# Kernel tuning notes

Measured on AMD Instinct MI355X. Metric: run time of the kernel, lower is better.

Reference implementation:

```python
import jax, jax.numpy as jnp
import numpy as np

THRESHOLD = 0.1  # matches init kwarg 'threshold'


def setup_inputs() -> dict:
    key = jax.random.key(0)
    ks = jax.random.split(key, 4)
    B, T, D = 16, 4096, 1024   # batch, tokens(=patch_h*patch_w), d_model
    E, R = 8, 64               # experts, lora rank
    inputs = jax.random.normal(ks[0], (B, T, D), dtype=jnp.float32)
    gate_w = jax.random.normal(ks[1], (D, E), dtype=jnp.float32) * (1.0 / np.sqrt(D))
    gate_b = jnp.zeros((E,), dtype=jnp.float32)
    lora_A = jax.random.normal(ks[2], (E, D, R), dtype=jnp.float32) * (1.0 / np.sqrt(D))
    lora_B = jax.random.normal(ks[3], (E, R, D), dtype=jnp.float32) * (1.0 / np.sqrt(R))
    return {"inputs": inputs, "gate_w": gate_w, "gate_b": gate_b,
            "lora_A": lora_A, "lora_B": lora_B, "patch_h": 64, "patch_w": 64}


def reference(inputs, gate_w, gate_b, lora_A, lora_B, patch_h, patch_w):
    # patch_h / patch_w are unused by 'linear' LoRA experts (kept for signature parity)
    D = inputs.shape[-1]
    x = inputs.reshape(-1, D)                                  # [N, D]
    gate_logits = jax.nn.softmax(x @ gate_w + gate_b, axis=-1)  # [N, E]
    selected = (gate_logits >= THRESHOLD).astype(x.dtype)       # threshold gate
    weights = gate_logits * selected
    wsum = jnp.sum(weights, axis=-1, keepdims=True)
    wsum = jnp.where(wsum == 0, jnp.ones_like(wsum), wsum)
    weights = weights / wsum                                    # renormalized weights [N, E]
    # Dense equivalent of per-expert gather/scatter: tokens with weight 0 contribute nothing,
    # identical to the boolean-indexed accumulation in the torch code.
    h = jnp.einsum('nd,edr->ner', x, lora_A)                    # [N, E, R]
    out = jnp.einsum('ner,erd,ne->nd', h, lora_B, weights)      # weighted combine [N, D]
    return out.reshape(inputs.shape[:-1] + (D,))
```

## Files before the change

kernel.cpp:

```cpp
#include <hip/hip_runtime.h>
#include <stdint.h>
#include <stddef.h>


typedef float f32x4 __attribute__((ext_vector_type(4)));
typedef short bf16x8 __attribute__((ext_vector_type(8)));

#define MFMA_16x16x32(A, B, C) __builtin_amdgcn_mfma_f32_16x16x32_bf16((A), (B), (C), 0, 0, 0)
#define SCHED_FENCE() __builtin_amdgcn_sched_barrier(0)
#define BAR() __builtin_amdgcn_s_barrier()
#define WAIT_LGKM0() asm volatile("s_waitcnt lgkmcnt(0)" ::: "memory")
#define WAIT_VM3() asm volatile("s_waitcnt vmcnt(3)" ::: "memory")
#define WAIT_VM0_LGKM0() asm volatile("s_waitcnt vmcnt(0) lgkmcnt(0)" ::: "memory")
#define WAIT_VM0() asm volatile("s_waitcnt vmcnt(0)" ::: "memory")

__device__ __forceinline__ unsigned short f2bf(float f) {
    union { float f; unsigned int u; } v;
    v.f = f;
    unsigned int u = v.u;
    u += 0x7FFFu + ((u >> 16) & 1u);
    return (unsigned short)(u >> 16);
}

__device__ __forceinline__ void load16_lds(unsigned short* lds, const unsigned short* g) {
    __builtin_amdgcn_global_load_lds(
        (const __attribute__((address_space(1))) unsigned int*)g,
        (__attribute__((address_space(3))) unsigned int*)lds, 16, 0, 0);
}

__global__ __launch_bounds__(256) void convert_pack(
        const float* __restrict__ LA, const float* __restrict__ LB,
        unsigned short* __restrict__ A_P, unsigned short* __restrict__ B_P) {
    int gid = blockIdx.x * 256 + threadIdx.x;
    if (gid < 524288) {
        int j = gid & 7, l = (gid >> 3) & 63, cblk = (gid >> 9) & 31, kblk = gid >> 14;
        int d = kblk * 32 + (l >> 4) * 8 + j;
        int col = cblk * 16 + (l & 15);
        int e = col >> 6, r = col & 63;
        A_P[gid] = f2bf(LA[((size_t)e * 1024 + d) * 64 + r]);
    } else {
        int idx = gid - 524288;
        int j = idx & 7, l = (idx >> 3) & 63, cblk = (idx >> 9) & 63, kblk = idx >> 15;
        int k = kblk * 32 + (l >> 4) * 8 + j;
        int d = cblk * 16 + (l & 15);
        int e = k >> 6, r = k & 63;
        B_P[idx] = f2bf(LB[((size_t)e * 64 + r) * 1024 + d]);
    }
}

__global__ __launch_bounds__(256) void gate_kernel(
        const float* __restrict__ X, const float* __restrict__ GW,
        const float* __restrict__ GB, float* __restrict__ Wg) {
    __shared__ float gwt[8 * 1024];
    int tid = threadIdx.x;

    {
        float r[4][8];
#pragma unroll
        for (int j = 0; j < 4; ++j) {
            const f32x4* gp = (const f32x4*)(GW + (size_t)(tid * 4 + j) * 8);
            f32x4 g0 = gp[0], g1 = gp[1];
#pragma unroll
            for (int q = 0; q < 4; ++q) { r[j][q] = g0[q]; r[j][4 + q] = g1[q]; }
        }
#pragma unroll
        for (int e = 0; e < 8; ++e) {
            f32x4 v;
#pragma unroll
            for (int j = 0; j < 4; ++j) v[j] = r[j][e];
            *(f32x4*)&gwt[e * 1024 + tid * 4] = v;
        }
    }
    __syncthreads();

    int row = blockIdx.x * 16 + (tid >> 4);
    int sub = tid & 15;
    const float* xr = X + (size_t)row * 1024 + sub * 4;
    float lg[8];
#pragma unroll
    for (int e = 0; e < 8; ++e) lg[e] = 0.f;
#pragma unroll 4
    for (int it = 0; it < 16; ++it) {
        f32x4 x = *(const f32x4*)(xr + it * 64);
#pragma unroll
        for (int e = 0; e < 8; ++e) {
            f32x4 g = *(const f32x4*)&gwt[e * 1024 + it * 64 + sub * 4];
            lg[e] += x[0] * g[0];
            lg[e] += x[1] * g[1];
            lg[e] += x[2] * g[2];
            lg[e] += x[3] * g[3];
        }
    }
#pragma unroll
    for (int s = 1; s < 16; s <<= 1) {
#pragma unroll
        for (int e = 0; e < 8; ++e) lg[e] += __shfl_xor(lg[e], s, 16);
    }
    float p[8], m = -1e30f, ssum = 0.f;
#pragma unroll
    for (int e = 0; e < 8; ++e) { lg[e] += GB[e]; m = fmaxf(m, lg[e]); }
#pragma unroll
    for (int e = 0; e < 8; ++e) { p[e] = expf(lg[e] - m); ssum += p[e]; }
    float inv = 1.f / ssum;
    float wv[8], wsum = 0.f;
#pragma unroll
    for (int e = 0; e < 8; ++e) {
        float pe = p[e] * inv;
        wv[e] = (pe >= 0.1f) ? pe : 0.f;
        wsum += wv[e];
    }
    if (wsum == 0.f) wsum = 1.f;
    float invw = 1.f / wsum;
    if (sub < 8) Wg[(size_t)row * 8 + sub] = wv[sub] * invw;
}

__global__ __launch_bounds__(512, 4) void stage1_kernel(
        const float* __restrict__ X, const unsigned short* __restrict__ A_P,
        const float* __restrict__ Wg, unsigned short* __restrict__ H_P) {
    __shared__ union SM1 {
        struct {
            unsigned short a[2][32 * 512];
            unsigned short x[2][64 * 40];
        } p;
        unsigned short hb[64 * 520];
    } sm;
    __shared__ float wl[512];

    int tid = threadIdx.x;
    int lane = tid & 63;
    int w = tid >> 6;
    int blk = blockIdx.x;
    int row = tid >> 3;
    int sub = tid & 7;

    wl[tid] = Wg[(size_t)blk * 512 + tid];

    const float* xp = X + (size_t)blk * 64 * 1024 + (size_t)row * 1024 + sub * 4;
    unsigned short* aCur = sm.p.a[0];
    unsigned short* aNxt = sm.p.a[1];
    unsigned short* xCur = sm.p.x[0];
    unsigned short* xNxt = sm.p.x[1];

    {
        const unsigned short* asrc = A_P + tid * 8;
#pragma unroll
        for (int i = 0; i < 4; ++i)
            load16_lds(&aCur[tid * 8 + i * 4096], asrc + i * 4096);
    }
    SCHED_FENCE();
    f32x4 xv0 = *(const f32x4*)(xp);
    f32x4 xv_hold = *(const f32x4*)(xp + 32);
    {
        unsigned int lo = (unsigned int)f2bf(xv0[0]) | ((unsigned int)f2bf(xv0[1]) << 16);
        unsigned int hi = (unsigned int)f2bf(xv0[2]) | ((unsigned int)f2bf(xv0[3]) << 16);
        *((uint2*)&xCur[row * 40 + sub * 4]) = make_uint2(lo, hi);
    }

    f32x4 acc[4][4] = {};
    for (int kb = 0; kb < 31; ++kb) {
        const unsigned short* asrc = A_P + (size_t)(kb + 1) * 16384 + tid * 8;
#pragma unroll
        for (int i = 0; i < 4; ++i)
            load16_lds(&aNxt[tid * 8 + i * 4096], asrc + i * 4096);
        SCHED_FENCE();
        int kbn = (kb + 2 <= 31) ? kb + 2 : 31;
        f32x4 xv_new = *(const f32x4*)(xp + (size_t)kbn * 32);
        unsigned int lo = (unsigned int)f2bf(xv_hold[0]) | ((unsigned int)f2bf(xv_hold[1]) << 16);
        unsigned int hi = (unsigned int)f2bf(xv_hold[2]) | ((unsigned int)f2bf(xv_hold[3]) << 16);
        *((uint2*)&xNxt[row * 40 + sub * 4]) = make_uint2(lo, hi);
        WAIT_LGKM0();
        SCHED_FENCE();
        BAR();
        SCHED_FENCE();
        bf16x8 af[4], bv[4];
#pragma unroll
        for (int m = 0; m < 4; ++m)
            af[m] = *(const bf16x8*)&xCur[(m * 16 + (lane & 15)) * 40 + (lane >> 4) * 8];
#pragma unroll
        for (int n = 0; n < 4; ++n)
            bv[n] = *(const bf16x8*)&aCur[(w * 4 + n) * 512 + lane * 8];
#pragma unroll
        for (int m = 0; m < 4; ++m)
#pragma unroll
            for (int n = 0; n < 4; ++n)
                acc[m][n] = MFMA_16x16x32(af[m], bv[n], acc[m][n]);
        BAR();
        unsigned short* t;
        t = aCur; aCur = aNxt; aNxt = t;
        t = xCur; xCur = xNxt; xNxt = t;
        xv_hold = xv_new;
    }
    WAIT_VM0_LGKM0();
    SCHED_FENCE();
    BAR();
    SCHED_FENCE();
    {
        bf16x8 af[4], bv[4];
#pragma unroll
        for (int m = 0; m < 4; ++m)
            af[m] = *(const bf16x8*)&xCur[(m * 16 + (lane & 15)) * 40 + (lane >> 4) * 8];
#pragma unroll
        for (int n = 0; n < 4; ++n)
            bv[n] = *(const bf16x8*)&aCur[(w * 4 + n) * 512 + lane * 8];
#pragma unroll
        for (int m = 0; m < 4; ++m)
#pragma unroll
            for (int n = 0; n < 4; ++n)
                acc[m][n] = MFMA_16x16x32(af[m], bv[n], acc[m][n]);
    }
    __syncthreads();

#pragma unroll
    for (int m = 0; m < 4; ++m) {
        float wv[4];
#pragma unroll
        for (int r = 0; r < 4; ++r)
            wv[r] = wl[(m * 16 + (lane >> 4) * 4 + r) * 8 + w];
#pragma unroll
        for (int n = 0; n < 4; ++n) {
            int col = w * 64 + n * 16 + (lane & 15);
#pragma unroll
            for (int r = 0; r < 4; ++r) {
                int rr = m * 16 + (lane >> 4) * 4 + r;
                sm.hb[rr * 520 + col] = f2bf(acc[m][n][r] * wv[r]);
            }
        }
    }
    __syncthreads();
#pragma unroll
    for (int it = 0; it < 8; ++it) {
        int gi = tid + it * 512;
        int ft = gi >> 6;
        int l2 = gi & 63;
        int rowblk = ft >> 4;
        int kblk = ft & 15;
        int rr = rowblk * 16 + (l2 & 15);
        int cs = kblk * 32 + (l2 >> 4) * 8;
        uint4 v = *(const uint4*)&sm.hb[rr * 520 + cs];
        *(uint4*)&H_P[(((size_t)blk * 4 + rowblk) * 16 + kblk) * 512 + l2 * 8] = v;
    }
}

__global__ __launch_bounds__(512, 4) void stage2_kernel(
        const unsigned short* __restrict__ H_P, const unsigned short* __restrict__ B_P,
        float* __restrict__ Out) {
    __shared__ unsigned short a_lds[2][8 * 512];
    __shared__ unsigned short b_lds[2][16 * 512];

    int tid = threadIdx.x;
    int lane = tid & 63;
    int wid = tid >> 6;
    int wr = wid >> 2, wc = wid & 3;
    int bw = blockIdx.x;
    int mt = ((bw >> 5) << 3) | (bw & 7);
    int nt = (bw >> 3) & 3;

    unsigned short* aCur = a_lds[0];
    unsigned short* aNxt = a_lds[1];
    unsigned short* bCur = b_lds[0];
    unsigned short* bNxt = b_lds[1];

    const unsigned short* hbase = H_P + ((size_t)mt * 8 + wid) * 16 * 512 + lane * 8;
    const unsigned short* bbase = B_P + (size_t)nt * 16 * 512 + tid * 8;

    load16_lds(&aCur[tid * 8], hbase);
    load16_lds(&bCur[tid * 8], bbase);
    load16_lds(&bCur[tid * 8 + 4096], bbase + 4096);

    f32x4 acc[4][4] = {};
    for (int kc = 0; kc < 15; ++kc) {
        load16_lds(&aNxt[tid * 8], hbase + (size_t)(kc + 1) * 512);
        load16_lds(&bNxt[tid * 8], bbase + (size_t)(kc + 1) * 32768);
        load16_lds(&bNxt[tid * 8 + 4096], bbase + (size_t)(kc + 1) * 32768 + 4096);
        WAIT_VM3();
        SCHED_FENCE();
        BAR();
        SCHED_FENCE();
        bf16x8 af[4], bv[4];
#pragma unroll
        for (int m = 0; m < 4; ++m)
            af[m] = *(const bf16x8*)&aCur[(wr * 4 + m) * 512 + lane * 8];
#pragma unroll
        for (int n = 0; n < 4; ++n)
            bv[n] = *(const bf16x8*)&bCur[(wc * 4 + n) * 512 + lane * 8];
#pragma unroll
        for (int m = 0; m < 4; ++m)
#pragma unroll
            for (int n = 0; n < 4; ++n)
                acc[m][n] = MFMA_16x16x32(af[m], bv[n], acc[m][n]);
        BAR();
        unsigned short* t;
        t = aCur; aCur = aNxt; aNxt = t;
        t = bCur; bCur = bNxt; bNxt = t;
    }
    WAIT_VM0();
    SCHED_FENCE();
    BAR();
    SCHED_FENCE();
    {
        bf16x8 af[4], bv[4];
#pragma unroll
        for (int m = 0; m < 4; ++m)
            af[m] = *(const bf16x8*)&aCur[(wr * 4 + m) * 512 + lane * 8];
#pragma unroll
        for (int n = 0; n < 4; ++n)
            bv[n] = *(const bf16x8*)&bCur[(wc * 4 + n) * 512 + lane * 8];
#pragma unroll
        for (int m = 0; m < 4; ++m)
#pragma unroll
            for (int n = 0; n < 4; ++n)
                acc[m][n] = MFMA_16x16x32(af[m], bv[n], acc[m][n]);
    }

    size_t rb = (size_t)mt * 128 + wr * 64;
    int cb = nt * 256 + wc * 64;
#pragma unroll
    for (int m = 0; m < 4; ++m)
#pragma unroll
        for (int n = 0; n < 4; ++n) {
            int col = cb + n * 16 + (lane & 15);
#pragma unroll
            for (int r = 0; r < 4; ++r) {
                size_t rrow = rb + m * 16 + (lane >> 4) * 4 + r;
                Out[rrow * 1024 + col] = acc[m][n][r];
            }
        }
}

extern "C" void kernel_launch(void* const* d_in, const int* in_sizes, int n_in,
                              void* d_out, int out_size, void* d_ws, size_t ws_size,
                              hipStream_t stream) {
    const float* X  = (const float*)d_in[0];
    const float* GW = (const float*)d_in[1];
    const float* GB = (const float*)d_in[2];
    const float* LA = (const float*)d_in[3];
    const float* LB = (const float*)d_in[4];
    float* Out = (float*)d_out;

    char* ws = (char*)d_ws;
    float*          Wg  = (float*)ws;
    unsigned short* A_P = (unsigned short*)(ws + (2u << 20));
    unsigned short* B_P = (unsigned short*)(ws + (3u << 20));
    unsigned short* H_P = (unsigned short*)(ws + (4u << 20));

    convert_pack<<<4096, 256, 0, stream>>>(LA, LB, A_P, B_P);
    gate_kernel<<<4096, 256, 0, stream>>>(X, GW, GB, Wg);
    stage1_kernel<<<1024, 512, 0, stream>>>(X, A_P, Wg, H_P);
    stage2_kernel<<<2048, 512, 0, stream>>>(H_P, B_P, Out);
}
```

Measured before the change: 302.5 us.

## Emit bf16 copy of X in gate kernel and feed stage1 via direct LDS loads

The gate kernel, which already streams X in fp32, now also writes a bf16 copy of X to workspace. A new stage1 variant reads that bf16 X with global_load_lds straight into a double-buffered LDS tile, so it no longer re-reads fp32 X and converts it in registers. This halves stage1's X read traffic and shortens its inner loop, at the cost of an extra 128 MB write in the gate kernel. The path is only taken when the workspace is large enough, otherwise the old fp32 path runs.

```diff
diff --git a/kernel.cpp b/kernel.cpp
--- a/kernel.cpp
+++ b/kernel.cpp
@@ -10,6 +10,8 @@
 #define SCHED_FENCE() __builtin_amdgcn_sched_barrier(0)
 #define BAR() __builtin_amdgcn_s_barrier()
 #define WAIT_LGKM0() asm volatile("s_waitcnt lgkmcnt(0)" ::: "memory")
+#define WAIT_VM5() asm volatile("s_waitcnt vmcnt(5)" ::: "memory")
+#define WAIT_VM4() asm volatile("s_waitcnt vmcnt(4)" ::: "memory")
 #define WAIT_VM3() asm volatile("s_waitcnt vmcnt(3)" ::: "memory")
 #define WAIT_VM0_LGKM0() asm volatile("s_waitcnt vmcnt(0) lgkmcnt(0)" ::: "memory")
 #define WAIT_VM0() asm volatile("s_waitcnt vmcnt(0)" ::: "memory")
@@ -48,9 +50,11 @@
     }
 }
 
+template<bool WX>
 __global__ __launch_bounds__(256) void gate_kernel(
         const float* __restrict__ X, const float* __restrict__ GW,
-        const float* __restrict__ GB, float* __restrict__ Wg) {
+        const float* __restrict__ GB, float* __restrict__ Wg,
+        unsigned short* __restrict__ Xbf) {
     __shared__ float gwt[8 * 1024];
     int tid = threadIdx.x;
 
@@ -82,6 +86,11 @@
 #pragma unroll 4
     for (int it = 0; it < 16; ++it) {
         f32x4 x = *(const f32x4*)(xr + it * 64);
+        if (WX) {
+            unsigned int lo = (unsigned int)f2bf(x[0]) | ((unsigned int)f2bf(x[1]) << 16);
+            unsigned int hi = (unsigned int)f2bf(x[2]) | ((unsigned int)f2bf(x[3]) << 16);
+            *(uint2*)(Xbf + (size_t)row * 1024 + it * 64 + sub * 4) = make_uint2(lo, hi);
+        }
 #pragma unroll
         for (int e = 0; e < 8; ++e) {
             f32x4 g = *(const f32x4*)&gwt[e * 1024 + it * 64 + sub * 4];
@@ -114,7 +123,104 @@
     if (sub < 8) Wg[(size_t)row * 8 + sub] = wv[sub] * invw;
 }
 
-__global__ __launch_bounds__(512, 4) void stage1_kernel(
+__global__ __launch_bounds__(512, 4) void stage1_bf(
+        const unsigned short* __restrict__ Xbf, const unsigned short* __restrict__ A_P,
+        const float* __restrict__ Wg, unsigned short* __restrict__ H_P) {
+    __shared__ union SM1 {
+        struct {
+            unsigned short a[2][16384];
+            unsigned short x[2][2048];
+        } p;
+        unsigned short hb[64 * 520];
+    } sm;
+    __shared__ float wl[512];
+
+    int tid = threadIdx.x;
+    int lane = tid & 63;
+    int w = tid >> 6;
+    int blk = blockIdx.x;
+
+    wl[tid] = Wg[(size_t)blk * 512 + tid];
+
+    const unsigned short* xsrc =
+        Xbf + ((size_t)blk * 64 + (w & 3) * 16 + (lane & 15)) * 1024 + (lane >> 4) * 8;
+
+    int cur = 0;
+    {
+        const unsigned short* asrc = A_P + tid * 8;
+#pragma unroll
+        for (int i = 0; i < 4; ++i)
+            load16_lds(&sm.p.a[0][tid * 8 + i * 4096], asrc + i * 4096);
+        if (w < 4)
+            load16_lds(&sm.p.x[0][w * 512 + lane * 8], xsrc);
+    }
+
+    f32x4 acc[4][4] = {};
+    for (int kb = 0; kb < 32; ++kb) {
+        if (kb < 31) {
+            const unsigned short* asrc = A_P + (size_t)(kb + 1) * 16384 + tid * 8;
+#pragma unroll
+            for (int i = 0; i < 4; ++i)
+                load16_lds(&sm.p.a[cur ^ 1][tid * 8 + i * 4096], asrc + i * 4096);
+            if (w < 4)
+                load16_lds(&sm.p.x[cur ^ 1][w * 512 + lane * 8], xsrc + (size_t)(kb + 1) * 32);
+            SCHED_FENCE();
+            if (w < 4) { WAIT_VM5(); } else { WAIT_VM4(); }
+        } else {
+            WAIT_VM0();
+        }
+        SCHED_FENCE();
+        BAR();
+        SCHED_FENCE();
+        bf16x8 af[4], bv[4];
+#pragma unroll
+        for (int m = 0; m < 4; ++m)
+            af[m] = *(const bf16x8*)&sm.p.x[cur][m * 512 + lane * 8];
+#pragma unroll
+        for (int n = 0; n < 4; ++n)
+            bv[n] = *(const bf16x8*)&sm.p.a[cur][(w * 4 + n) * 512 + lane * 8];
+#pragma unroll
+        for (int m = 0; m < 4; ++m)
+#pragma unroll
+            for (int n = 0; n < 4; ++n)
+                acc[m][n] = MFMA_16x16x32(af[m], bv[n], acc[m][n]);
+        BAR();
+        cur ^= 1;
+    }
+    __syncthreads();
+
+#pragma unroll
+    for (int m = 0; m < 4; ++m) {
+        float wv[4];
+#pragma unroll
+        for (int r = 0; r < 4; ++r)
+            wv[r] = wl[(m * 16 + (lane >> 4) * 4 + r) * 8 + w];
+#pragma unroll
+        for (int n = 0; n < 4; ++n) {
+            int col = w * 64 + n * 16 + (lane & 15);
+#pragma unroll
+            for (int r = 0; r < 4; ++r) {
+                int rr = m * 16 + (lane >> 4) * 4 + r;
+                sm.hb[rr * 520 + col] = f2bf(acc[m][n][r] * wv[r]);
+            }
+        }
+    }
+    __syncthreads();
+#pragma unroll
+    for (int it = 0; it < 8; ++it) {
+        int gi = tid + it * 512;
+        int ft = gi >> 6;
+        int l2 = gi & 63;
+        int rowblk = ft >> 4;
+        int kblk = ft & 15;
+        int rr = rowblk * 16 + (l2 & 15);
+        int cs = kblk * 32 + (l2 >> 4) * 8;
+        uint4 v = *(const uint4*)&sm.hb[rr * 520 + cs];
+        *(uint4*)&H_P[(((size_t)blk * 4 + rowblk) * 16 + kblk) * 512 + l2 * 8] = v;
+    }
+}
+
+__global__ __launch_bounds__(512, 4) void stage1_f32(
         const float* __restrict__ X, const unsigned short* __restrict__ A_P,
         const float* __restrict__ Wg, unsigned short* __restrict__ H_P) {
     __shared__ union SM1 {
@@ -342,9 +448,17 @@
     unsigned short* A_P = (unsigned short*)(ws + (2u << 20));
     unsigned short* B_P = (unsigned short*)(ws + (3u << 20));
     unsigned short* H_P = (unsigned short*)(ws + (4u << 20));
+    unsigned short* Xbf = (unsigned short*)(ws + (68u << 20));
+
+    bool big = ws_size >= ((size_t)196 << 20);
 
     convert_pack<<<4096, 256, 0, stream>>>(LA, LB, A_P, B_P);
-    gate_kernel<<<4096, 256, 0, stream>>>(X, GW, GB, Wg);
-    stage1_kernel<<<1024, 512, 0, stream>>>(X, A_P, Wg, H_P);
+    if (big) {
+        gate_kernel<true><<<4096, 256, 0, stream>>>(X, GW, GB, Wg, Xbf);
+        stage1_bf<<<1024, 512, 0, stream>>>(Xbf, A_P, Wg, H_P);
+    } else {
+        gate_kernel<false><<<4096, 256, 0, stream>>>(X, GW, GB, Wg, nullptr);
+        stage1_f32<<<1024, 512, 0, stream>>>(X, A_P, Wg, H_P);
+    }
     stage2_kernel<<<2048, 512, 0, stream>>>(H_P, B_P, Out);
 }
```

Result: slower. 314.0 us (+3.8%).

## Fuse stage1 and stage2 so H stays in LDS, preload gate inputs

Applied to the files above, without the earlier changes.

Merges the two GEMM stages into one kernel. The weighted bf16 H tile stays in shared memory and each wave multiplies it directly against B_P, reading B fragments straight from global memory. This removes the H_P round trip through global memory and one launch. The cost is that the second GEMM loses its double-buffered LDS staging for B, and each block re-reads all of B_P from global or L2. Separately, the gate kernel now loads all X chunks into registers up front and batches the gwt LDS reads, which exposes more memory parallelism but uses more registers.

```diff
diff --git a/kernel.cpp b/kernel.cpp
--- a/kernel.cpp
+++ b/kernel.cpp
@@ -10,9 +10,7 @@
 #define SCHED_FENCE() __builtin_amdgcn_sched_barrier(0)
 #define BAR() __builtin_amdgcn_s_barrier()
 #define WAIT_LGKM0() asm volatile("s_waitcnt lgkmcnt(0)" ::: "memory")
-#define WAIT_VM3() asm volatile("s_waitcnt vmcnt(3)" ::: "memory")
 #define WAIT_VM0_LGKM0() asm volatile("s_waitcnt vmcnt(0) lgkmcnt(0)" ::: "memory")
-#define WAIT_VM0() asm volatile("s_waitcnt vmcnt(0)" ::: "memory")
 
 __device__ __forceinline__ unsigned short f2bf(float f) {
     union { float f; unsigned int u; } v;
@@ -76,19 +74,28 @@
     int row = blockIdx.x * 16 + (tid >> 4);
     int sub = tid & 15;
     const float* xr = X + (size_t)row * 1024 + sub * 4;
+
+    f32x4 xs[16];
+#pragma unroll
+    for (int it = 0; it < 16; ++it) xs[it] = *(const f32x4*)(xr + it * 64);
+
     float lg[8];
 #pragma unroll
     for (int e = 0; e < 8; ++e) lg[e] = 0.f;
-#pragma unroll 4
+
+#pragma unroll
     for (int it = 0; it < 16; ++it) {
-        f32x4 x = *(const f32x4*)(xr + it * 64);
+        f32x4 g[8];
+#pragma unroll
+        for (int e = 0; e < 8; ++e)
+            g[e] = *(const f32x4*)&gwt[e * 1024 + it * 64 + sub * 4];
+        f32x4 x = xs[it];
 #pragma unroll
         for (int e = 0; e < 8; ++e) {
-            f32x4 g = *(const f32x4*)&gwt[e * 1024 + it * 64 + sub * 4];
-            lg[e] += x[0] * g[0];
-            lg[e] += x[1] * g[1];
-            lg[e] += x[2] * g[2];
-            lg[e] += x[3] * g[3];
+            lg[e] += x[0] * g[e][0];
+            lg[e] += x[1] * g[e][1];
+            lg[e] += x[2] * g[e][2];
+            lg[e] += x[3] * g[e][3];
         }
     }
 #pragma unroll
@@ -114,9 +121,10 @@
     if (sub < 8) Wg[(size_t)row * 8 + sub] = wv[sub] * invw;
 }
 
-__global__ __launch_bounds__(512, 4) void stage1_kernel(
+__global__ __launch_bounds__(512, 4) void fused_kernel(
         const float* __restrict__ X, const unsigned short* __restrict__ A_P,
-        const float* __restrict__ Wg, unsigned short* __restrict__ H_P) {
+        const unsigned short* __restrict__ B_P, const float* __restrict__ Wg,
+        float* __restrict__ Out) {
     __shared__ union SM1 {
         struct {
             unsigned short a[2][32 * 512];
@@ -227,104 +235,39 @@
         }
     }
     __syncthreads();
-#pragma unroll
-    for (int it = 0; it < 8; ++it) {
-        int gi = tid + it * 512;
-        int ft = gi >> 6;
-        int l2 = gi & 63;
-        int rowblk = ft >> 4;
-        int kblk = ft & 15;
-        int rr = rowblk * 16 + (l2 & 15);
-        int cs = kblk * 32 + (l2 >> 4) * 8;
-        uint4 v = *(const uint4*)&sm.hb[rr * 520 + cs];
-        *(uint4*)&H_P[(((size_t)blk * 4 + rowblk) * 16 + kblk) * 512 + l2 * 8] = v;
-    }
-}
-
-__global__ __launch_bounds__(512, 4) void stage2_kernel(
-        const unsigned short* __restrict__ H_P, const unsigned short* __restrict__ B_P,
-        float* __restrict__ Out) {
-    __shared__ unsigned short a_lds[2][8 * 512];
-    __shared__ unsigned short b_lds[2][16 * 512];
-
-    int tid = threadIdx.x;
-    int lane = tid & 63;
-    int wid = tid >> 6;
-    int wr = wid >> 2, wc = wid & 3;
-    int bw = blockIdx.x;
-    int mt = ((bw >> 5) << 3) | (bw & 7);
-    int nt = (bw >> 3) & 3;
-
-    unsigned short* aCur = a_lds[0];
-    unsigned short* aNxt = a_lds[1];
-    unsigned short* bCur = b_lds[0];
-    unsigned short* bNxt = b_lds[1];
-
-    const unsigned short* hbase = H_P + ((size_t)mt * 8 + wid) * 16 * 512 + lane * 8;
-    const unsigned short* bbase = B_P + (size_t)nt * 16 * 512 + tid * 8;
-
-    load16_lds(&aCur[tid * 8], hbase);
-    load16_lds(&bCur[tid * 8], bbase);
-    load16_lds(&bCur[tid * 8 + 4096], bbase + 4096);
-
-    f32x4 acc[4][4] = {};
-    for (int kc = 0; kc < 15; ++kc) {
-        load16_lds(&aNxt[tid * 8], hbase + (size_t)(kc + 1) * 512);
-        load16_lds(&bNxt[tid * 8], bbase + (size_t)(kc + 1) * 32768);
-        load16_lds(&bNxt[tid * 8 + 4096], bbase + (size_t)(kc + 1) * 32768 + 4096);
-        WAIT_VM3();
-        SCHED_FENCE();
-        BAR();
-        SCHED_FENCE();
-        bf16x8 af[4], bv[4];
-#pragma unroll
-        for (int m = 0; m < 4; ++m)
-            af[m] = *(const bf16x8*)&aCur[(wr * 4 + m) * 512 + lane * 8];
-#pragma unroll
-        for (int n = 0; n < 4; ++n)
-            bv[n] = *(const bf16x8*)&bCur[(wc * 4 + n) * 512 + lane * 8];
-#pragma unroll
-        for (int m = 0; m < 4; ++m)
+
+#pragma unroll
+    for (int h = 0; h < 2; ++h) {
+        f32x4 acc2[4][4] = {};
+        int cb0 = w * 8 + h * 4;
+        for (int kc = 0; kc < 16; ++kc) {
+            bf16x8 af2[4], bv2[4];
 #pragma unroll
             for (int n = 0; n < 4; ++n)
-                acc[m][n] = MFMA_16x16x32(af[m], bv[n], acc[m][n]);
-        BAR();
-        unsigned short* t;
-        t = aCur; aCur = aNxt; aNxt = t;
-        t = bCur; bCur = bNxt; bNxt = t;
-    }
-    WAIT_VM0();
-    SCHED_FENCE();
-    BAR();
-    SCHED_FENCE();
-    {
-        bf16x8 af[4], bv[4];
-#pragma unroll
-        for (int m = 0; m < 4; ++m)
-            af[m] = *(const bf16x8*)&aCur[(wr * 4 + m) * 512 + lane * 8];
-#pragma unroll
-        for (int n = 0; n < 4; ++n)
-            bv[n] = *(const bf16x8*)&bCur[(wc * 4 + n) * 512 + lane * 8];
-#pragma unroll
-        for (int m = 0; m < 4; ++m)
-#pragma unroll
-            for (int n = 0; n < 4; ++n)
-                acc[m][n] = MFMA_16x16x32(af[m], bv[n], acc[m][n]);
-    }
-
-    size_t rb = (size_t)mt * 128 + wr * 64;
-    int cb = nt * 256 + wc * 64;
-#pragma unroll
-    for (int m = 0; m < 4; ++m)
-#pragma unroll
-        for (int n = 0; n < 4; ++n) {
-            int col = cb + n * 16 + (lane & 15);
-#pragma unroll
-            for (int r = 0; r < 4; ++r) {
-                size_t rrow = rb + m * 16 + (lane >> 4) * 4 + r;
-                Out[rrow * 1024 + col] = acc[m][n][r];
+                bv2[n] = *(const bf16x8*)(B_P + (((size_t)kc * 64 + cb0 + n) * 64 + lane) * 8);
+#pragma unroll
+            for (int m = 0; m < 4; ++m)
+                af2[m] = *(const bf16x8*)&sm.hb[(m * 16 + (lane & 15)) * 520 + kc * 32 + (lane >> 4) * 8];
+#pragma unroll
+            for (int m = 0; m < 4; ++m)
+#pragma unroll
+                for (int n = 0; n < 4; ++n)
+                    acc2[m][n] = MFMA_16x16x32(af2[m], bv2[n], acc2[m][n]);
+        }
+        size_t rb = (size_t)blk * 64;
+        int cb = w * 128 + h * 64;
+#pragma unroll
+        for (int m = 0; m < 4; ++m)
+#pragma unroll
+            for (int n = 0; n < 4; ++n) {
+                int col = cb + n * 16 + (lane & 15);
+#pragma unroll
+                for (int r = 0; r < 4; ++r) {
+                    size_t rrow = rb + m * 16 + (lane >> 4) * 4 + r;
+                    Out[rrow * 1024 + col] = acc2[m][n][r];
+                }
             }
-        }
+    }
 }
 
 extern "C" void kernel_launch(void* const* d_in, const int* in_sizes, int n_in,
@@ -341,10 +284,8 @@
     float*          Wg  = (float*)ws;
     unsigned short* A_P = (unsigned short*)(ws + (2u << 20));
     unsigned short* B_P = (unsigned short*)(ws + (3u << 20));
-    unsigned short* H_P = (unsigned short*)(ws + (4u << 20));
 
     convert_pack<<<4096, 256, 0, stream>>>(LA, LB, A_P, B_P);
     gate_kernel<<<4096, 256, 0, stream>>>(X, GW, GB, Wg);
-    stage1_kernel<<<1024, 512, 0, stream>>>(X, A_P, Wg, H_P);
-    stage2_kernel<<<2048, 512, 0, stream>>>(H_P, B_P, Out);
-}
+    fused_kernel<<<1024, 512, 0, stream>>>(X, A_P, B_P, Wg, Out);
+}
```

New measurement: 310.2 us. 1.03x slower.
